# Kernel optimization log

Hardware: AMD Instinct MI355X
Metric: run time of the kernel (lower is better)

The kernel has to match this reference:

```python
import jax, jax.numpy as jnp
import numpy as np

B = 128
N = 512            # num_nodes
RU = 64            # rnn_units = hidden_size // num_nodes
IN_PER_NODE = 2    # input_size // num_nodes
MEM_DIM = 16
BOT_DIM = 4
IN_SZ = IN_PER_NODE + RU      # 66, concat(input, state) per node
OUT_SZ = 4 * RU               # 256, 4 LSTM gates


def setup_inputs() -> dict:
    key = jax.random.key(0)
    ks = jax.random.split(key, 12)
    std = 1.0 / np.sqrt(N * RU)  # reset_parameters: uniform(-std, std)
    u = lambda k, shape: jax.random.uniform(k, shape, jnp.float32, -std, std)
    return {
        "inputs": jax.random.normal(ks[0], (B, N * IN_PER_NODE), jnp.float32),
        "hx": jax.random.normal(ks[1], (B, N * RU), jnp.float32),
        "cx": jax.random.normal(ks[2], (B, N * RU), jnp.float32),
        "memory": u(ks[3], (N, MEM_DIM)),
        "w1": u(ks[4], (MEM_DIM, MEM_DIM)),
        "b1": u(ks[5], (MEM_DIM,)),
        "w2": u(ks[6], (MEM_DIM, BOT_DIM)),
        "b2": u(ks[7], (BOT_DIM,)),
        "w3": u(ks[8], (BOT_DIM, IN_SZ * OUT_SZ)),
        "b3": u(ks[9], (IN_SZ * OUT_SZ,)),
        "b_out": u(ks[10], (OUT_SZ,)),
    }


def reference(inputs, hx, cx, memory, w1, b1, w2, b2, w3, b3, b_out):
    b = inputs.shape[0]
    n = memory.shape[0]
    ru = hx.shape[1] // n
    # per-node concat of input and state: [B, N, IN_SZ]
    x = inputs.reshape(b, n, -1)
    h = hx.reshape(b, n, ru)
    xs = jnp.concatenate([x, h], axis=-1)
    # hypernetwork: memory -> per-node weight matrices [N, IN_SZ, OUT_SZ]
    mem = jnp.tanh(memory @ w1 + b1)
    mem = jnp.tanh(mem @ w2 + b2)
    W = (mem @ w3 + b3).reshape(n, xs.shape[-1], -1)
    # batched per-node matmul (original repeats W over batch; same math without the repeat)
    val = jax.nn.sigmoid(jnp.einsum('bni,nio->bno', xs, W)) + b_out  # [B, N, 4*RU]
    g = val.reshape(b, n, 4, ru)
    i_t = jax.nn.sigmoid(g[:, :, 0, :].reshape(b, n * ru))
    f_t = jax.nn.sigmoid(g[:, :, 1, :].reshape(b, n * ru))
    g_t = jnp.tanh(g[:, :, 2, :].reshape(b, n * ru))
    o_t = jax.nn.sigmoid(g[:, :, 3, :].reshape(b, n * ru))
    cy = cx * f_t + i_t * g_t
    hy = o_t * jnp.tanh(cy)
    return hy, cy
```

## Files before the change

kernel.cpp:

```cpp
#include <hip/hip_runtime.h>
#include <math.h>

#define BATCH 128
#define NNODE 512
#define RU 64
#define MEM_DIM 16
#define BOT_DIM 4
#define IN_SZ 66
#define OUT_SZ 256
#define HID (NNODE*RU)
#define W3_ROW 16896
#define W5_BYTES (240*512*2)

typedef __attribute__((ext_vector_type(8))) short short8;
typedef __attribute__((ext_vector_type(4))) float float4v;

__device__ __forceinline__ unsigned short f2bf(float f) {
    unsigned int u = __float_as_uint(f);
    unsigned int r = (u + 0x7FFFu + ((u >> 16) & 1u)) >> 16;
    return (unsigned short)r;
}
__device__ __forceinline__ float fsig(float x) {
    return __builtin_amdgcn_rcpf(1.0f + __expf(-x));
}
__device__ __forceinline__ float ftanh(float x) {
    return 1.0f - 2.0f * __builtin_amdgcn_rcpf(1.0f + __expf(2.0f * x));
}

__global__ __launch_bounds__(256) void prep_kernel(
    const float* __restrict__ memory, const float* __restrict__ w1,
    const float* __restrict__ b1,     const float* __restrict__ w2,
    const float* __restrict__ b2,     const float* __restrict__ w3,
    const float* __restrict__ b3,     unsigned short* __restrict__ W5,
    float* __restrict__ m2_ws)
{
    const int tid = threadIdx.x;
    const int bid = blockIdx.x;
    if (bid < 60) {
        const int c    = bid * 256 + tid;
        const int lane = c & 63;
        const int f    = c >> 6;
        const int ks   = f % 3;
        const int t2   = f / 3;
        const int ct   = t2 & 15;
        const int k    = t2 >> 4;
        const int q = lane & 15, quad = lane >> 4;
        const int o = (ct & 3) * 64 + (ct >> 2) * 16 + q;
        const float* src = (k < 4) ? (w3 + k * W3_ROW) : b3;
        short8 v;
        #pragma unroll
        for (int j = 0; j < 8; ++j) {
            const int s = ks * 32 + quad * 8 + j;
            float x = 0.f;
            if (s < IN_SZ) {
                const int i = (s < 64) ? s + 2 : s - 64;
                x = src[i * OUT_SZ + o];
            }
            v[j] = (short)f2bf(x);
        }
        *(short8*)(W5 + f * 512 + lane * 8) = v;
    } else {
        const int n = (bid - 60) * 256 + tid;
        if (n < NNODE) {
            float memv[MEM_DIM];
            #pragma unroll
            for (int j = 0; j < MEM_DIM; ++j) memv[j] = memory[n * MEM_DIM + j];
            float mem1[MEM_DIM];
            #pragma unroll
            for (int t = 0; t < MEM_DIM; ++t) {
                float s = b1[t];
                #pragma unroll
                for (int j = 0; j < MEM_DIM; ++j) s += memv[j] * w1[j * MEM_DIM + t];
                mem1[t] = ftanh(s);
            }
            #pragma unroll
            for (int t = 0; t < BOT_DIM; ++t) {
                float s = b2[t];
                #pragma unroll
                for (int j = 0; j < MEM_DIM; ++j) s += mem1[j] * w2[j * BOT_DIM + t];
                m2_ws[n * 4 + t] = ftanh(s);
            }
        }
    }
}

__global__ __launch_bounds__(512, 2) void fused_kernel(
    const float* __restrict__ inputs, const float* __restrict__ hx,
    const float* __restrict__ cx,     const float* __restrict__ b_out,
    const unsigned short* __restrict__ W5, const float* __restrict__ m2_ws,
    float* __restrict__ out)
{
    const int tid  = threadIdx.x;
    const int n    = blockIdx.x;
    const int w    = tid >> 6;
    const int lane = tid & 63;
    const int rh   = w >> 2;
    const int qh   = w & 3;
    const int q    = lane & 15;
    const int quad = lane >> 4;

    float coef[5];
    #pragma unroll
    for (int k = 0; k < 4; ++k) coef[k] = m2_ws[n * 4 + k];
    coef[4] = 1.0f;

    float4v xa[4][4];
    float xin[4][2];
    #pragma unroll
    for (int rt = 0; rt < 4; ++rt) {
        const int row = rh * 64 + rt * 16 + q;
        const float* hrow = hx + (size_t)row * HID + n * RU + quad * 8;
        xa[rt][0] = *(const float4v*)(hrow);
        xa[rt][1] = *(const float4v*)(hrow + 4);
        xa[rt][2] = *(const float4v*)(hrow + 32);
        xa[rt][3] = *(const float4v*)(hrow + 36);
        if (quad == 0) {
            const float* ip = inputs + (size_t)row * (NNODE * 2) + n * 2;
            xin[rt][0] = ip[0];
            xin[rt][1] = ip[1];
        } else {
            xin[rt][0] = 0.f;
            xin[rt][1] = 0.f;
        }
    }

    const int r = qh * 16 + q;
    float bo[4];
    #pragma unroll
    for (int g = 0; g < 4; ++g) bo[g] = b_out[g * 64 + r];
    float cxr[4][4];
    #pragma unroll
    for (int rt = 0; rt < 4; ++rt)
        #pragma unroll
        for (int v = 0; v < 4; ++v) {
            const int b = rh * 64 + rt * 16 + quad * 4 + v;
            cxr[rt][v] = cx[(size_t)b * HID + n * RU + r];
        }

    float4v acc[4][4];
    #pragma unroll
    for (int rt = 0; rt < 4; ++rt)
        #pragma unroll
        for (int g = 0; g < 4; ++g)
            acc[rt][g] = (float4v){0.f, 0.f, 0.f, 0.f};

    #pragma unroll
    for (int k = 0; k < 5; ++k) {
        const float cf = coef[k];
        short8 af[3][4];
        #pragma unroll
        for (int rt = 0; rt < 4; ++rt) {
            #pragma unroll
            for (int ksh = 0; ksh < 2; ++ksh) {
                float4v lo = xa[rt][ksh * 2];
                float4v hi = xa[rt][ksh * 2 + 1];
                if (k < 4) { lo *= cf; hi *= cf; }
                short8 t;
                t[0] = (short)f2bf(lo[0]); t[1] = (short)f2bf(lo[1]);
                t[2] = (short)f2bf(lo[2]); t[3] = (short)f2bf(lo[3]);
                t[4] = (short)f2bf(hi[0]); t[5] = (short)f2bf(hi[1]);
                t[6] = (short)f2bf(hi[2]); t[7] = (short)f2bf(hi[3]);
                af[ksh][rt] = t;
            }
            float a0 = xin[rt][0], a1 = xin[rt][1];
            if (k < 4) { a0 *= cf; a1 *= cf; }
            short8 t2 = {0, 0, 0, 0, 0, 0, 0, 0};
            t2[0] = (short)f2bf(a0);
            t2[1] = (short)f2bf(a1);
            af[2][rt] = t2;
        }
        #pragma unroll
        for (int ks = 0; ks < 3; ++ks)
            #pragma unroll
            for (int g = 0; g < 4; ++g) {
                const short8 bf = *(const short8*)(
                    W5 + (size_t)((k * 16 + qh * 4 + g) * 3 + ks) * 512 + lane * 8);
                #pragma unroll
                for (int rt = 0; rt < 4; ++rt)
                    acc[rt][g] = __builtin_amdgcn_mfma_f32_16x16x32_bf16(
                        af[ks][rt], bf, acc[rt][g], 0, 0, 0);
            }
    }

    #pragma unroll
    for (int rt = 0; rt < 4; ++rt) {
        #pragma unroll
        for (int v = 0; v < 4; ++v) {
            const int b = rh * 64 + rt * 16 + quad * 4 + v;
            const size_t idx = (size_t)b * HID + n * RU + r;
            float vi = fsig(acc[rt][0][v]) + bo[0];
            float vf = fsig(acc[rt][1][v]) + bo[1];
            float vg = fsig(acc[rt][2][v]) + bo[2];
            float vo = fsig(acc[rt][3][v]) + bo[3];
            float it = fsig(vi), ft = fsig(vf);
            float gt = ftanh(vg), ot = fsig(vo);
            float cc = cxr[rt][v] * ft + it * gt;
            out[idx] = ot * ftanh(cc);
            out[(size_t)BATCH * HID + idx] = cc;
        }
    }
}

extern "C" void kernel_launch(void* const* d_in, const int* in_sizes, int n_in,
                              void* d_out, int out_size, void* d_ws, size_t ws_size,
                              hipStream_t stream) {
    const float* inputs = (const float*)d_in[0];
    const float* hx     = (const float*)d_in[1];
    const float* cx     = (const float*)d_in[2];
    const float* memory = (const float*)d_in[3];
    const float* w1     = (const float*)d_in[4];
    const float* b1     = (const float*)d_in[5];
    const float* w2     = (const float*)d_in[6];
    const float* b2     = (const float*)d_in[7];
    const float* w3     = (const float*)d_in[8];
    const float* b3     = (const float*)d_in[9];
    const float* b_out  = (const float*)d_in[10];
    float* out = (float*)d_out;

    unsigned short* W5 = (unsigned short*)d_ws;
    float* m2_ws = (float*)((char*)d_ws + W5_BYTES);

    prep_kernel<<<62, 256, 0, stream>>>(memory, w1, b1, w2, b2, w3, b3, W5, m2_ws);
    fused_kernel<<<NNODE, 512, 0, stream>>>(inputs, hx, cx, b_out, W5, m2_ws, out);
}
```

Before: 138.1 us.

## Materialize per-node weights in LDS and split each node across two blocks

Instead of running five MFMA passes with the input scaled by each hypernetwork coefficient, each block now builds the node's combined weight slice (sum of coef_k*w3_k plus b3) in fp32 from a pre-laid-out fp32 workspace. It converts the slice to bf16 in shared memory and runs a single MFMA pass. This cuts MFMA work and activation conversions by about five times. Each node is split over two 256-thread blocks covering half the output columns, which raises the block count. The cost is reading fp32 weight planes per block from L2 (the workspace doubles in size), some redundant hx loads across the two half-blocks, and a slight change in rounding.

```diff
diff --git a/kernel.cpp b/kernel.cpp
--- a/kernel.cpp
+++ b/kernel.cpp
@@ -10,7 +10,8 @@
 #define OUT_SZ 256
 #define HID (NNODE*RU)
 #define W3_ROW 16896
-#define W5_BYTES (240*512*2)
+#define W5F_FLOATS (240*512)
+#define K_STEP 24576
 
 typedef __attribute__((ext_vector_type(8))) short short8;
 typedef __attribute__((ext_vector_type(4))) float float4v;
@@ -31,36 +32,39 @@
     const float* __restrict__ memory, const float* __restrict__ w1,
     const float* __restrict__ b1,     const float* __restrict__ w2,
     const float* __restrict__ b2,     const float* __restrict__ w3,
-    const float* __restrict__ b3,     unsigned short* __restrict__ W5,
+    const float* __restrict__ b3,     float* __restrict__ W5f,
     float* __restrict__ m2_ws)
 {
     const int tid = threadIdx.x;
     const int bid = blockIdx.x;
-    if (bid < 60) {
-        const int c    = bid * 256 + tid;
-        const int lane = c & 63;
-        const int f    = c >> 6;
-        const int ks   = f % 3;
-        const int t2   = f / 3;
-        const int ct   = t2 & 15;
-        const int k    = t2 >> 4;
+    if (bid < 120) {
+        const int id = bid * 256 + tid;
+        const int F  = id * 4;
+        const int f  = F >> 9;
+        const int r  = F & 511;
+        const int lane = r >> 3;
+        const int j0   = r & 7;
+        const int ks = f % 3;
+        const int t2 = f / 3;
+        const int ct = t2 & 15;
+        const int k  = t2 >> 4;
         const int q = lane & 15, quad = lane >> 4;
         const int o = (ct & 3) * 64 + (ct >> 2) * 16 + q;
         const float* src = (k < 4) ? (w3 + k * W3_ROW) : b3;
-        short8 v;
-        #pragma unroll
-        for (int j = 0; j < 8; ++j) {
-            const int s = ks * 32 + quad * 8 + j;
+        float4v v;
+        #pragma unroll
+        for (int jj = 0; jj < 4; ++jj) {
+            const int s = ks * 32 + quad * 8 + j0 + jj;
             float x = 0.f;
             if (s < IN_SZ) {
                 const int i = (s < 64) ? s + 2 : s - 64;
                 x = src[i * OUT_SZ + o];
             }
-            v[j] = (short)f2bf(x);
-        }
-        *(short8*)(W5 + f * 512 + lane * 8) = v;
+            v[jj] = x;
+        }
+        *(float4v*)(W5f + F) = v;
     } else {
-        const int n = (bid - 60) * 256 + tid;
+        const int n = (bid - 120) * 256 + tid;
         if (n < NNODE) {
             float memv[MEM_DIM];
             #pragma unroll
@@ -84,31 +88,31 @@
     }
 }
 
-__global__ __launch_bounds__(512, 2) void fused_kernel(
+__global__ __launch_bounds__(256, 3) void fused_kernel(
     const float* __restrict__ inputs, const float* __restrict__ hx,
     const float* __restrict__ cx,     const float* __restrict__ b_out,
-    const unsigned short* __restrict__ W5, const float* __restrict__ m2_ws,
+    const float* __restrict__ W5f,    const float* __restrict__ m2_ws,
     float* __restrict__ out)
 {
+    __shared__ unsigned short Wl[24 * 512];
     const int tid  = threadIdx.x;
-    const int n    = blockIdx.x;
+    const unsigned bid = blockIdx.x;
+    const int n    = bid >> 1;
+    const int h    = bid & 1;
     const int w    = tid >> 6;
     const int lane = tid & 63;
-    const int rh   = w >> 2;
-    const int qh   = w & 3;
     const int q    = lane & 15;
     const int quad = lane >> 4;
 
-    float coef[5];
+    float coef[4];
     #pragma unroll
     for (int k = 0; k < 4; ++k) coef[k] = m2_ws[n * 4 + k];
-    coef[4] = 1.0f;
-
-    float4v xa[4][4];
-    float xin[4][2];
-    #pragma unroll
-    for (int rt = 0; rt < 4; ++rt) {
-        const int row = rh * 64 + rt * 16 + q;
+
+    float4v xa[2][4];
+    float xin[2][2];
+    #pragma unroll
+    for (int rt = 0; rt < 2; ++rt) {
+        const int row = w * 32 + rt * 16 + q;
         const float* hrow = hx + (size_t)row * HID + n * RU + quad * 8;
         xa[rt][0] = *(const float4v*)(hrow);
         xa[rt][1] = *(const float4v*)(hrow + 4);
@@ -124,79 +128,105 @@
         }
     }
 
-    const int r = qh * 16 + q;
-    float bo[4];
-    #pragma unroll
-    for (int g = 0; g < 4; ++g) bo[g] = b_out[g * 64 + r];
-    float cxr[4][4];
-    #pragma unroll
-    for (int rt = 0; rt < 4; ++rt)
+    #pragma unroll
+    for (int it = 0; it < 6; ++it) {
+        const int c  = it * 256 + tid;
+        const int fl = c >> 6;
+        const int l  = c & 63;
+        const int ctl = fl / 3;
+        const int ks  = fl - ctl * 3;
+        const float* p = W5f + (size_t)(((h * 8 + ctl) * 3 + ks) * 512) + l * 8;
+        float4v r0 = *(const float4v*)(p + 4 * K_STEP);
+        float4v r1 = *(const float4v*)(p + 4 * K_STEP + 4);
+        #pragma unroll
+        for (int k = 0; k < 4; ++k) {
+            r0 += coef[k] * *(const float4v*)(p + k * K_STEP);
+            r1 += coef[k] * *(const float4v*)(p + k * K_STEP + 4);
+        }
+        short8 ov;
+        ov[0] = (short)f2bf(r0[0]); ov[1] = (short)f2bf(r0[1]);
+        ov[2] = (short)f2bf(r0[2]); ov[3] = (short)f2bf(r0[3]);
+        ov[4] = (short)f2bf(r1[0]); ov[5] = (short)f2bf(r1[1]);
+        ov[6] = (short)f2bf(r1[2]); ov[7] = (short)f2bf(r1[3]);
+        *(short8*)(Wl + fl * 512 + l * 8) = ov;
+    }
+
+    float bo[2][4];
+    #pragma unroll
+    for (int rh = 0; rh < 2; ++rh)
+        #pragma unroll
+        for (int g = 0; g < 4; ++g)
+            bo[rh][g] = b_out[g * 64 + (h * 2 + rh) * 16 + q];
+
+    float cxr[2][4][2];
+    #pragma unroll
+    for (int rt = 0; rt < 2; ++rt)
         #pragma unroll
         for (int v = 0; v < 4; ++v) {
-            const int b = rh * 64 + rt * 16 + quad * 4 + v;
-            cxr[rt][v] = cx[(size_t)b * HID + n * RU + r];
-        }
-
-    float4v acc[4][4];
-    #pragma unroll
-    for (int rt = 0; rt < 4; ++rt)
-        #pragma unroll
-        for (int g = 0; g < 4; ++g)
-            acc[rt][g] = (float4v){0.f, 0.f, 0.f, 0.f};
-
-    #pragma unroll
-    for (int k = 0; k < 5; ++k) {
-        const float cf = coef[k];
-        short8 af[3][4];
-        #pragma unroll
-        for (int rt = 0; rt < 4; ++rt) {
-            #pragma unroll
-            for (int ksh = 0; ksh < 2; ++ksh) {
-                float4v lo = xa[rt][ksh * 2];
-                float4v hi = xa[rt][ksh * 2 + 1];
-                if (k < 4) { lo *= cf; hi *= cf; }
-                short8 t;
-                t[0] = (short)f2bf(lo[0]); t[1] = (short)f2bf(lo[1]);
-                t[2] = (short)f2bf(lo[2]); t[3] = (short)f2bf(lo[3]);
-                t[4] = (short)f2bf(hi[0]); t[5] = (short)f2bf(hi[1]);
-                t[6] = (short)f2bf(hi[2]); t[7] = (short)f2bf(hi[3]);
-                af[ksh][rt] = t;
-            }
-            float a0 = xin[rt][0], a1 = xin[rt][1];
-            if (k < 4) { a0 *= cf; a1 *= cf; }
-            short8 t2 = {0, 0, 0, 0, 0, 0, 0, 0};
-            t2[0] = (short)f2bf(a0);
-            t2[1] = (short)f2bf(a1);
-            af[2][rt] = t2;
-        }
-        #pragma unroll
-        for (int ks = 0; ks < 3; ++ks)
-            #pragma unroll
-            for (int g = 0; g < 4; ++g) {
-                const short8 bf = *(const short8*)(
-                    W5 + (size_t)((k * 16 + qh * 4 + g) * 3 + ks) * 512 + lane * 8);
-                #pragma unroll
-                for (int rt = 0; rt < 4; ++rt)
-                    acc[rt][g] = __builtin_amdgcn_mfma_f32_16x16x32_bf16(
-                        af[ks][rt], bf, acc[rt][g], 0, 0, 0);
-            }
-    }
-
-    #pragma unroll
-    for (int rt = 0; rt < 4; ++rt) {
+            const int b = w * 32 + rt * 16 + quad * 4 + v;
+            #pragma unroll
+            for (int rh = 0; rh < 2; ++rh)
+                cxr[rt][v][rh] = cx[(size_t)b * HID + n * RU + (h * 2 + rh) * 16 + q];
+        }
+
+    short8 a[3][2];
+    #pragma unroll
+    for (int rt = 0; rt < 2; ++rt) {
+        #pragma unroll
+        for (int ksh = 0; ksh < 2; ++ksh) {
+            float4v lo = xa[rt][ksh * 2];
+            float4v hi = xa[rt][ksh * 2 + 1];
+            short8 t;
+            t[0] = (short)f2bf(lo[0]); t[1] = (short)f2bf(lo[1]);
+            t[2] = (short)f2bf(lo[2]); t[3] = (short)f2bf(lo[3]);
+            t[4] = (short)f2bf(hi[0]); t[5] = (short)f2bf(hi[1]);
+            t[6] = (short)f2bf(hi[2]); t[7] = (short)f2bf(hi[3]);
+            a[ksh][rt] = t;
+        }
+        short8 t2 = {0, 0, 0, 0, 0, 0, 0, 0};
+        t2[0] = (short)f2bf(xin[rt][0]);
+        t2[1] = (short)f2bf(xin[rt][1]);
+        a[2][rt] = t2;
+    }
+
+    float4v acc[2][8];
+    #pragma unroll
+    for (int rt = 0; rt < 2; ++rt)
+        #pragma unroll
+        for (int ctl = 0; ctl < 8; ++ctl)
+            acc[rt][ctl] = (float4v){0.f, 0.f, 0.f, 0.f};
+
+    __syncthreads();
+
+    #pragma unroll
+    for (int ks = 0; ks < 3; ++ks) {
+        #pragma unroll
+        for (int ctl = 0; ctl < 8; ++ctl) {
+            short8 bf = *(const short8*)(Wl + (ctl * 3 + ks) * 512 + lane * 8);
+            acc[0][ctl] = __builtin_amdgcn_mfma_f32_16x16x32_bf16(a[ks][0], bf, acc[0][ctl], 0, 0, 0);
+            acc[1][ctl] = __builtin_amdgcn_mfma_f32_16x16x32_bf16(a[ks][1], bf, acc[1][ctl], 0, 0, 0);
+        }
+    }
+
+    #pragma unroll
+    for (int rt = 0; rt < 2; ++rt) {
         #pragma unroll
         for (int v = 0; v < 4; ++v) {
-            const int b = rh * 64 + rt * 16 + quad * 4 + v;
-            const size_t idx = (size_t)b * HID + n * RU + r;
-            float vi = fsig(acc[rt][0][v]) + bo[0];
-            float vf = fsig(acc[rt][1][v]) + bo[1];
-            float vg = fsig(acc[rt][2][v]) + bo[2];
-            float vo = fsig(acc[rt][3][v]) + bo[3];
-            float it = fsig(vi), ft = fsig(vf);
-            float gt = ftanh(vg), ot = fsig(vo);
-            float cc = cxr[rt][v] * ft + it * gt;
-            out[idx] = ot * ftanh(cc);
-            out[(size_t)BATCH * HID + idx] = cc;
+            const int b = w * 32 + rt * 16 + quad * 4 + v;
+            const size_t base = (size_t)b * HID + n * RU;
+            #pragma unroll
+            for (int rh = 0; rh < 2; ++rh) {
+                float vi = fsig(acc[rt][rh * 4 + 0][v]) + bo[rh][0];
+                float vf = fsig(acc[rt][rh * 4 + 1][v]) + bo[rh][1];
+                float vg = fsig(acc[rt][rh * 4 + 2][v]) + bo[rh][2];
+                float vo = fsig(acc[rt][rh * 4 + 3][v]) + bo[rh][3];
+                float it = fsig(vi), ft = fsig(vf);
+                float gt = ftanh(vg), ot = fsig(vo);
+                const size_t idx = base + (h * 2 + rh) * 16 + q;
+                float cc = cxr[rt][v][rh] * ft + it * gt;
+                out[idx] = ot * ftanh(cc);
+                out[(size_t)BATCH * HID + idx] = cc;
+            }
         }
     }
 }
@@ -217,9 +247,9 @@
     const float* b_out  = (const float*)d_in[10];
     float* out = (float*)d_out;
 
-    unsigned short* W5 = (unsigned short*)d_ws;
-    float* m2_ws = (float*)((char*)d_ws + W5_BYTES);
-
-    prep_kernel<<<62, 256, 0, stream>>>(memory, w1, b1, w2, b2, w3, b3, W5, m2_ws);
-    fused_kernel<<<NNODE, 512, 0, stream>>>(inputs, hx, cx, b_out, W5, m2_ws, out);
-}
+    float* W5f   = (float*)d_ws;
+    float* m2_ws = (float*)((char*)d_ws + W5F_FLOATS * 4);
+
+    prep_kernel<<<122, 256, 0, stream>>>(memory, w1, b1, w2, b2, w3, b3, W5f, m2_ws);
+    fused_kernel<<<NNODE * 2, 256, 0, stream>>>(inputs, hx, cx, b_out, W5f, m2_ws, out);
+}
```

After: 126.8 us. -8.2%, faster.
